# Performance work log

Hardware: AMD Instinct MI355X
Metric: run time of the kernel (lower is better)

Reference implementation:

```python
import jax, jax.numpy as jnp
import numpy as np

N_NODES = 100000
N_EDGES = 1000000
IN_CH = 64
HID = 64
NUM_GRAPHS = 1024


def gcn_conv(x, edge_index, W, b):
    # GCNConv with self-loops and symmetric normalization.
    src, dst = edge_index[0], edge_index[1]
    n = x.shape[0]
    # degree including self-loop
    deg = jax.ops.segment_sum(jnp.ones(src.shape[0], x.dtype), dst, num_segments=n) + 1.0
    dinv = jax.lax.rsqrt(deg)
    xw = x @ W  # [N, out]
    norm = dinv[src] * dinv[dst]  # per-edge 1/sqrt(d_i d_j)
    msg = xw[src] * norm[:, None]  # [E, out] gather + scale
    agg = jax.ops.segment_sum(msg, dst, num_segments=n)
    # self-loop contribution: norm = 1/deg
    return agg + xw / deg[:, None] + b


def setup_inputs() -> dict:
    key = jax.random.key(0)
    k = jax.random.split(key, 8)
    x = jax.random.normal(k[0], (N_NODES, IN_CH), dtype=jnp.float32)
    edge_index = jax.random.randint(k[1], (2, N_EDGES), 0, N_NODES, dtype=jnp.int64)
    batch = jnp.sort(jax.random.randint(k[2], (N_NODES,), 0, NUM_GRAPHS, dtype=jnp.int64))
    s1 = 1.0 / np.sqrt(IN_CH)
    s2 = 1.0 / np.sqrt(HID)
    W1 = jax.random.uniform(k[3], (IN_CH, HID), jnp.float32, -s1, s1)
    b1 = jnp.zeros((HID,), jnp.float32)
    W2 = jax.random.uniform(k[4], (HID, HID), jnp.float32, -s2, s2)
    b2 = jnp.zeros((HID,), jnp.float32)
    Wout = jax.random.uniform(k[5], (HID, 1), jnp.float32, -s2, s2)
    bout = jnp.zeros((1,), jnp.float32)
    return {"x": x, "edge_index": edge_index, "batch": batch,
            "W1": W1, "b1": b1, "W2": W2, "b2": b2, "Wout": Wout, "bout": bout}


def reference(x, edge_index, batch, W1, b1, W2, b2, Wout, bout):
    h = jax.nn.relu(gcn_conv(x, edge_index, W1, b1))
    h = jax.nn.relu(gcn_conv(h, edge_index, W2, b2))
    # global_mean_pool over batch ids
    sums = jax.ops.segment_sum(h, batch, num_segments=NUM_GRAPHS)
    cnt = jax.ops.segment_sum(jnp.ones(h.shape[0], h.dtype), batch, num_segments=NUM_GRAPHS)
    pooled = sums / jnp.maximum(cnt, 1.0)[:, None]  # [G, HID]
    return (pooled @ Wout + bout).reshape(-1)
```

## Files before the change

kernel.cpp:

```cpp
#include <hip/hip_runtime.h>
#include <hip/hip_fp16.h>

#define N_NODES   100000
#define N_EDGES   1000000
#define NPAIR     (N_NODES / 2)
#define HID       64
#define NUM_GRAPHS 1024
#define NREP      8
#define CAP       32
#define PPW       8

typedef _Float16 h16;

static __device__ __forceinline__ int pack2(float a, float b) {
    union { h16 h[2]; int i; } u;
    u.h[0] = (h16)a; u.h[1] = (h16)b;
    return u.i;
}


__global__ __launch_bounds__(256) void bucket_fill(const int* __restrict__ src,
                                                   const int* __restrict__ dst,
                                                   int* __restrict__ cnt,
                                                   int* __restrict__ ebuf) {
    int part  = blockIdx.x & 7;
    int e     = (blockIdx.x >> 3) * 256 + threadIdx.x;
    if (e >= N_EDGES) return;
    int d = dst[e];
    if (((d >> 7) & 7) != part) return;
    int p = atomicAdd(&cnt[d], 1);
    if (p < CAP) ebuf[(size_t)d * CAP + p] = src[e];
}


__global__ __launch_bounds__(256) void gemm64h(const float* __restrict__ X,
                                               const float* __restrict__ W,
                                               const int* __restrict__ cnt,
                                               h16* __restrict__ Y, int nrows) {
    __shared__ float Wl[4096];
    int t = threadIdx.x;
    #pragma unroll
    for (int i = 0; i < 4; i++) {
        int idx = (t + i * 256) * 4;
        *(float4*)(Wl + idx) = *(const float4*)(W + idx);
    }
    __syncthreads();
    int row  = blockIdx.x * 128 + (t >> 1);
    if (row >= nrows) return;
    int half = t & 1;
    float df = (float)(min(cnt[row], CAP) + 1);
    float sc = rsqrtf(df);
    const float4* xr = (const float4*)(X + (size_t)row * 64);
    float4 acc[8];
    #pragma unroll
    for (int j = 0; j < 8; j++) acc[j] = make_float4(0.f, 0.f, 0.f, 0.f);
    const float* wb = Wl + half * 32;
    #pragma unroll
    for (int k4 = 0; k4 < 16; k4++) {
        float4 xv = xr[k4];
        #pragma unroll
        for (int kk = 0; kk < 4; kk++) {
            float xk = (kk == 0) ? xv.x : (kk == 1) ? xv.y : (kk == 2) ? xv.z : xv.w;
            const float4* wr = (const float4*)(wb + (k4 * 4 + kk) * 64);
            #pragma unroll
            for (int j = 0; j < 8; j++) {
                float4 wv = wr[j];
                acc[j].x += xk * wv.x;
                acc[j].y += xk * wv.y;
                acc[j].z += xk * wv.z;
                acc[j].w += xk * wv.w;
            }
        }
    }
    int4* yr = (int4*)(Y + (size_t)row * 64 + half * 32);
    #pragma unroll
    for (int j = 0; j < 4; j++) {
        float4 a = acc[2 * j], b = acc[2 * j + 1];
        int4 o;
        o.x = pack2(a.x * sc, a.y * sc); o.y = pack2(a.z * sc, a.w * sc);
        o.z = pack2(b.x * sc, b.y * sc); o.w = pack2(b.z * sc, b.w * sc);
        yr[j] = o;
    }
}


template <int U>
static __device__ __forceinline__ float agg_chunk(const h16* __restrict__ XW,
                                                  int es, int j, int lane) {
    int ss[U]; float vv[U];
    #pragma unroll
    for (int u = 0; u < U; u++) ss[u] = __builtin_amdgcn_readlane(es, j + u);
    #pragma unroll
    for (int u = 0; u < U; u++)
        vv[u] = (float)XW[(((unsigned)ss[u]) << 6) | (unsigned)lane];
    float a = 0.f;
    #pragma unroll
    for (int u = 0; u < U; u++) a += vv[u];
    return a;
}

static __device__ __forceinline__ float agg_edges(const h16* __restrict__ XW,
                                                  int es, int deg, int lane, int base) {
    float acc = 0.f;
    int j = 0;
    for (; j + 16 <= deg; j += 16) { acc += agg_chunk<16>(XW, es, base + j, lane); }
    if (deg & 8) { acc += agg_chunk<8>(XW, es, base + j, lane); j += 8; }
    if (deg & 4) { acc += agg_chunk<4>(XW, es, base + j, lane); j += 4; }
    if (deg & 2) { acc += agg_chunk<2>(XW, es, base + j, lane); j += 2; }
    if (deg & 1) { acc += agg_chunk<1>(XW, es, base + j, lane); }
    return acc;
}

__global__ __launch_bounds__(256) void agg_gemm_relu(const h16* __restrict__ XW,
                                                     const int* __restrict__ cnt,
                                                     const int* __restrict__ ebuf,
                                                     const float* __restrict__ bias,
                                                     const float* __restrict__ W2,
                                                     h16* __restrict__ Y2) {
    __shared__ float W2q[4096];
    __shared__ float hbuf[512];
    int t = threadIdx.x;
    #pragma unroll
    for (int i = 0; i < 16; i++) {
        int L = t + i * 256;
        int k = L >> 6, c = L & 63;
        W2q[(k >> 2) * 256 + c * 4 + (k & 3)] = W2[L];
    }
    __syncthreads();
    int lane = t & 63;
    int w = t >> 6;
    float* hb0 = hbuf + w * 128;
    float* hb1 = hb0 + 64;
    float bl = bias[lane];
    int gw = blockIdx.x * 4 + w;
    int p = gw * PPW;
    if (p >= NPAIR) return;
    int pend = min(p + PPW, NPAIR);
    int   es = ebuf[p * 64 + lane];
    float s0 = (float)XW[p * 128 + lane];
    float s1 = (float)XW[p * 128 + 64 + lane];
    int2  c2 = *(const int2*)(cnt + 2 * p);
    while (p < pend) {
        int pn = p + 1;
        int esn = 0; float s0n = 0.f, s1n = 0.f; int2 c2n = make_int2(0, 0);
        if (pn < pend) {
            esn = ebuf[pn * 64 + lane];
            s0n = (float)XW[pn * 128 + lane];
            s1n = (float)XW[pn * 128 + 64 + lane];
            c2n = *(const int2*)(cnt + 2 * pn);
        }
        int deg0 = min(__builtin_amdgcn_readfirstlane(c2.x), CAP);
        int deg1 = min(__builtin_amdgcn_readfirstlane(c2.y), CAP);
        float dv0 = rsqrtf((float)(deg0 + 1));
        float dv1 = rsqrtf((float)(deg1 + 1));
        float acc0 = s0 + agg_edges(XW, es, deg0, lane, 0);
        float acc1 = s1 + agg_edges(XW, es, deg1, lane, 32);
        float h0 = fmaxf(fmaf(dv0, acc0, bl), 0.f);
        float h1 = fmaxf(fmaf(dv1, acc1, bl), 0.f);
        hb0[lane] = h0;
        hb1[lane] = h1;
        float y0 = 0.f, y1 = 0.f;
        #pragma unroll
        for (int k4 = 0; k4 < 16; k4++) {
            float4 hp0 = *(const float4*)(hb0 + k4 * 4);
            float4 hp1 = *(const float4*)(hb1 + k4 * 4);
            float4 wq  = *(const float4*)(W2q + k4 * 256 + lane * 4);
            y0 = fmaf(hp0.x, wq.x, y0); y1 = fmaf(hp1.x, wq.x, y1);
            y0 = fmaf(hp0.y, wq.y, y0); y1 = fmaf(hp1.y, wq.y, y1);
            y0 = fmaf(hp0.z, wq.z, y0); y1 = fmaf(hp1.z, wq.z, y1);
            y0 = fmaf(hp0.w, wq.w, y0); y1 = fmaf(hp1.w, wq.w, y1);
        }
        Y2[p * 128 + lane]      = (h16)(y0 * dv0);
        Y2[p * 128 + 64 + lane] = (h16)(y1 * dv1);
        es = esn; s0 = s0n; s1 = s1n; c2 = c2n;
        p = pn;
    }
}

__global__ __launch_bounds__(256) void agg_pool(const h16* __restrict__ XW,
                                                const int* __restrict__ cnt,
                                                const int* __restrict__ ebuf,
                                                const float* __restrict__ bias,
                                                const float* __restrict__ Wout,
                                                const int* __restrict__ batch,
                                                float* __restrict__ outsum) {
    int t = threadIdx.x;
    int lane = t & 63;
    int w = t >> 6;
    float bl = bias[lane];
    float wl = Wout[lane];
    int gw = blockIdx.x * 4 + w;
    int p = gw * PPW;
    if (p >= NPAIR) return;
    int pend = min(p + PPW, NPAIR);
    int   es = ebuf[p * 64 + lane];
    float s0 = (float)XW[p * 128 + lane];
    float s1 = (float)XW[p * 128 + 64 + lane];
    int2  c2 = *(const int2*)(cnt + 2 * p);
    int2  b2 = *(const int2*)(batch + 2 * p);
    while (p < pend) {
        int pn = p + 1;
        int esn = 0; float s0n = 0.f, s1n = 0.f;
        int2 c2n = make_int2(0, 0), b2n = make_int2(0, 0);
        if (pn < pend) {
            esn = ebuf[pn * 64 + lane];
            s0n = (float)XW[pn * 128 + lane];
            s1n = (float)XW[pn * 128 + 64 + lane];
            c2n = *(const int2*)(cnt + 2 * pn);
            b2n = *(const int2*)(batch + 2 * pn);
        }
        int deg0 = min(__builtin_amdgcn_readfirstlane(c2.x), CAP);
        int deg1 = min(__builtin_amdgcn_readfirstlane(c2.y), CAP);
        float dv0 = rsqrtf((float)(deg0 + 1));
        float dv1 = rsqrtf((float)(deg1 + 1));
        float acc0 = s0 + agg_edges(XW, es, deg0, lane, 0);
        float acc1 = s1 + agg_edges(XW, es, deg1, lane, 32);
        float v0 = fmaxf(fmaf(dv0, acc0, bl), 0.f) * wl;
        float v1 = fmaxf(fmaf(dv1, acc1, bl), 0.f) * wl;
        #pragma unroll
        for (int off = 32; off > 0; off >>= 1) {
            v0 += __shfl_down(v0, off, 64);
            v1 += __shfl_down(v1, off, 64);
        }
        if (lane == 0) {
            atomicAdd(&outsum[((2 * p)     & (NREP - 1)) * NUM_GRAPHS + b2.x], v0);
            atomicAdd(&outsum[((2 * p + 1) & (NREP - 1)) * NUM_GRAPHS + b2.y], v1);
        }
        es = esn; s0 = s0n; s1 = s1n; c2 = c2n; b2 = b2n;
        p = pn;
    }
}

__global__ __launch_bounds__(256) void finalize(const float* __restrict__ outsum,
                                                const int* __restrict__ batch,
                                                const float* __restrict__ bout,
                                                float* __restrict__ out) {
    int g = blockIdx.x * 256 + threadIdx.x;
    if (g >= NUM_GRAPHS) return;
    float s = 0.f;
    #pragma unroll
    for (int r = 0; r < NREP; r++) s += outsum[r * NUM_GRAPHS + g];
    int lo = 0, hi = N_NODES;
    while (lo < hi) { int mid = (lo + hi) >> 1; if (batch[mid] <  g) lo = mid + 1; else hi = mid; }
    int lo2 = lo, hi2 = N_NODES;
    while (lo2 < hi2) { int mid = (lo2 + hi2) >> 1; if (batch[mid] <= g) lo2 = mid + 1; else hi2 = mid; }
    float c = (float)max(lo2 - lo, 1);
    out[g] = s / c + bout[0];
}


extern "C" void kernel_launch(void* const* d_in, const int* in_sizes, int n_in,
                              void* d_out, int out_size, void* d_ws, size_t ws_size,
                              hipStream_t stream) {
    const float* x     = (const float*)d_in[0];
    const int*   eidx  = (const int*)d_in[1];
    const int*   batch = (const int*)d_in[2];
    const float* W1    = (const float*)d_in[3];
    const float* b1    = (const float*)d_in[4];
    const float* W2    = (const float*)d_in[5];
    const float* b2    = (const float*)d_in[6];
    const float* Wout  = (const float*)d_in[7];
    const float* bout  = (const float*)d_in[8];
    float* out = (float*)d_out;

    const int* src = eidx;
    const int* dst = eidx + N_EDGES;

    h16*   xw     = (h16*)d_ws;
    h16*   y2     = xw + (size_t)N_NODES * 64;
    int*   ebuf   = (int*)(y2 + (size_t)N_NODES * 64);
    int*   cnt    = ebuf + (size_t)N_NODES * CAP;
    float* outsum = (float*)(cnt + N_NODES);

    hipMemsetAsync(cnt, 0, (size_t)(N_NODES + NREP * NUM_GRAPHS) * sizeof(int), stream);

    const int EB  = (N_EDGES + 255) / 256;
    const int GB  = (N_NODES + 127) / 128;
    const int AGB = (NPAIR + 4 * PPW - 1) / (4 * PPW);

    bucket_fill<<<EB * 8, 256, 0, stream>>>(src, dst, cnt, ebuf);
    gemm64h<<<GB, 256, 0, stream>>>(x, W1, cnt, xw, N_NODES);
    agg_gemm_relu<<<AGB, 256, 0, stream>>>(xw, cnt, ebuf, b1, W2, y2);
    agg_pool<<<AGB, 256, 0, stream>>>(y2, cnt, ebuf, b2, Wout, batch, outsum);
    finalize<<<(NUM_GRAPHS + 255) / 256, 256, 0, stream>>>(outsum, batch, bout, out);
}
```

Baseline: 244.1 us.

## Process two node pairs per wave without loop, and vectorize W2 staging

```diff
diff --git a/kernel.cpp b/kernel.cpp
--- a/kernel.cpp
+++ b/kernel.cpp
@@ -8,7 +8,6 @@
 #define NUM_GRAPHS 1024
 #define NREP      8
 #define CAP       32
-#define PPW       8
 
 typedef _Float16 h16;
 
@@ -118,63 +117,70 @@
                                                      const float* __restrict__ W2,
                                                      h16* __restrict__ Y2) {
     __shared__ float W2q[4096];
-    __shared__ float hbuf[512];
+    __shared__ float hbuf[1024];
     int t = threadIdx.x;
     #pragma unroll
-    for (int i = 0; i < 16; i++) {
-        int L = t + i * 256;
-        int k = L >> 6, c = L & 63;
-        W2q[(k >> 2) * 256 + c * 4 + (k & 3)] = W2[L];
+    for (int i = 0; i < 4; i++) {
+        int L0 = (t + i * 256) * 4;
+        float4 wv = *(const float4*)(W2 + L0);
+        int k = L0 >> 6, c = L0 & 63;
+        float* dp = &W2q[(k >> 2) * 256 + (k & 3)];
+        dp[(c + 0) * 4] = wv.x;
+        dp[(c + 1) * 4] = wv.y;
+        dp[(c + 2) * 4] = wv.z;
+        dp[(c + 3) * 4] = wv.w;
     }
     __syncthreads();
     int lane = t & 63;
     int w = t >> 6;
-    float* hb0 = hbuf + w * 128;
-    float* hb1 = hb0 + 64;
+    float* hb = hbuf + w * 256;
     float bl = bias[lane];
     int gw = blockIdx.x * 4 + w;
-    int p = gw * PPW;
-    if (p >= NPAIR) return;
-    int pend = min(p + PPW, NPAIR);
-    int   es = ebuf[p * 64 + lane];
-    float s0 = (float)XW[p * 128 + lane];
-    float s1 = (float)XW[p * 128 + 64 + lane];
-    int2  c2 = *(const int2*)(cnt + 2 * p);
-    while (p < pend) {
-        int pn = p + 1;
-        int esn = 0; float s0n = 0.f, s1n = 0.f; int2 c2n = make_int2(0, 0);
-        if (pn < pend) {
-            esn = ebuf[pn * 64 + lane];
-            s0n = (float)XW[pn * 128 + lane];
-            s1n = (float)XW[pn * 128 + 64 + lane];
-            c2n = *(const int2*)(cnt + 2 * pn);
-        }
-        int deg0 = min(__builtin_amdgcn_readfirstlane(c2.x), CAP);
-        int deg1 = min(__builtin_amdgcn_readfirstlane(c2.y), CAP);
-        float dv0 = rsqrtf((float)(deg0 + 1));
-        float dv1 = rsqrtf((float)(deg1 + 1));
-        float acc0 = s0 + agg_edges(XW, es, deg0, lane, 0);
-        float acc1 = s1 + agg_edges(XW, es, deg1, lane, 32);
-        float h0 = fmaxf(fmaf(dv0, acc0, bl), 0.f);
-        float h1 = fmaxf(fmaf(dv1, acc1, bl), 0.f);
-        hb0[lane] = h0;
-        hb1[lane] = h1;
-        float y0 = 0.f, y1 = 0.f;
-        #pragma unroll
-        for (int k4 = 0; k4 < 16; k4++) {
-            float4 hp0 = *(const float4*)(hb0 + k4 * 4);
-            float4 hp1 = *(const float4*)(hb1 + k4 * 4);
-            float4 wq  = *(const float4*)(W2q + k4 * 256 + lane * 4);
-            y0 = fmaf(hp0.x, wq.x, y0); y1 = fmaf(hp1.x, wq.x, y1);
-            y0 = fmaf(hp0.y, wq.y, y0); y1 = fmaf(hp1.y, wq.y, y1);
-            y0 = fmaf(hp0.z, wq.z, y0); y1 = fmaf(hp1.z, wq.z, y1);
-            y0 = fmaf(hp0.w, wq.w, y0); y1 = fmaf(hp1.w, wq.w, y1);
-        }
-        Y2[p * 128 + lane]      = (h16)(y0 * dv0);
-        Y2[p * 128 + 64 + lane] = (h16)(y1 * dv1);
-        es = esn; s0 = s0n; s1 = s1n; c2 = c2n;
-        p = pn;
-    }
+    int pA = gw * 2, pB = pA + 1;
+    int   esA = ebuf[pA * 64 + lane];
+    int   esB = ebuf[pB * 64 + lane];
+    float sA0 = (float)XW[pA * 128 + lane];
+    float sA1 = (float)XW[pA * 128 + 64 + lane];
+    float sB0 = (float)XW[pB * 128 + lane];
+    float sB1 = (float)XW[pB * 128 + 64 + lane];
+    int4  c4  = *(const int4*)(cnt + 4 * gw);
+    int dA0 = min(__builtin_amdgcn_readfirstlane(c4.x), CAP);
+    int dA1 = min(__builtin_amdgcn_readfirstlane(c4.y), CAP);
+    int dB0 = min(__builtin_amdgcn_readfirstlane(c4.z), CAP);
+    int dB1 = min(__builtin_amdgcn_readfirstlane(c4.w), CAP);
+    float vA0 = rsqrtf((float)(dA0 + 1));
+    float vA1 = rsqrtf((float)(dA1 + 1));
+    float vB0 = rsqrtf((float)(dB0 + 1));
+    float vB1 = rsqrtf((float)(dB1 + 1));
+    float a0 = sA0 + agg_edges(XW, esA, dA0, lane, 0);
+    float a1 = sA1 + agg_edges(XW, esA, dA1, lane, 32);
+    float a2 = sB0 + agg_edges(XW, esB, dB0, lane, 0);
+    float a3 = sB1 + agg_edges(XW, esB, dB1, lane, 32);
+    hb[lane]       = fmaxf(fmaf(vA0, a0, bl), 0.f);
+    hb[64 + lane]  = fmaxf(fmaf(vA1, a1, bl), 0.f);
+    hb[128 + lane] = fmaxf(fmaf(vB0, a2, bl), 0.f);
+    hb[192 + lane] = fmaxf(fmaf(vB1, a3, bl), 0.f);
+    float y0 = 0.f, y1 = 0.f, y2 = 0.f, y3 = 0.f;
+    #pragma unroll
+    for (int k4 = 0; k4 < 16; k4++) {
+        float4 wq = *(const float4*)(W2q + k4 * 256 + lane * 4);
+        float4 h0 = *(const float4*)(hb + k4 * 4);
+        float4 h1 = *(const float4*)(hb + 64 + k4 * 4);
+        float4 h2 = *(const float4*)(hb + 128 + k4 * 4);
+        float4 h3 = *(const float4*)(hb + 192 + k4 * 4);
+        y0 = fmaf(h0.x, wq.x, y0); y1 = fmaf(h1.x, wq.x, y1);
+        y2 = fmaf(h2.x, wq.x, y2); y3 = fmaf(h3.x, wq.x, y3);
+        y0 = fmaf(h0.y, wq.y, y0); y1 = fmaf(h1.y, wq.y, y1);
+        y2 = fmaf(h2.y, wq.y, y2); y3 = fmaf(h3.y, wq.y, y3);
+        y0 = fmaf(h0.z, wq.z, y0); y1 = fmaf(h1.z, wq.z, y1);
+        y2 = fmaf(h2.z, wq.z, y2); y3 = fmaf(h3.z, wq.z, y3);
+        y0 = fmaf(h0.w, wq.w, y0); y1 = fmaf(h1.w, wq.w, y1);
+        y2 = fmaf(h2.w, wq.w, y2); y3 = fmaf(h3.w, wq.w, y3);
+    }
+    Y2[pA * 128 + lane]       = (h16)(y0 * vA0);
+    Y2[pA * 128 + 64 + lane]  = (h16)(y1 * vA1);
+    Y2[pB * 128 + lane]       = (h16)(y2 * vB0);
+    Y2[pB * 128 + 64 + lane]  = (h16)(y3 * vB1);
 }
 
 __global__ __launch_bounds__(256) void agg_pool(const h16* __restrict__ XW,
@@ -190,44 +196,44 @@
     float bl = bias[lane];
     float wl = Wout[lane];
     int gw = blockIdx.x * 4 + w;
-    int p = gw * PPW;
-    if (p >= NPAIR) return;
-    int pend = min(p + PPW, NPAIR);
-    int   es = ebuf[p * 64 + lane];
-    float s0 = (float)XW[p * 128 + lane];
-    float s1 = (float)XW[p * 128 + 64 + lane];
-    int2  c2 = *(const int2*)(cnt + 2 * p);
-    int2  b2 = *(const int2*)(batch + 2 * p);
-    while (p < pend) {
-        int pn = p + 1;
-        int esn = 0; float s0n = 0.f, s1n = 0.f;
-        int2 c2n = make_int2(0, 0), b2n = make_int2(0, 0);
-        if (pn < pend) {
-            esn = ebuf[pn * 64 + lane];
-            s0n = (float)XW[pn * 128 + lane];
-            s1n = (float)XW[pn * 128 + 64 + lane];
-            c2n = *(const int2*)(cnt + 2 * pn);
-            b2n = *(const int2*)(batch + 2 * pn);
-        }
-        int deg0 = min(__builtin_amdgcn_readfirstlane(c2.x), CAP);
-        int deg1 = min(__builtin_amdgcn_readfirstlane(c2.y), CAP);
-        float dv0 = rsqrtf((float)(deg0 + 1));
-        float dv1 = rsqrtf((float)(deg1 + 1));
-        float acc0 = s0 + agg_edges(XW, es, deg0, lane, 0);
-        float acc1 = s1 + agg_edges(XW, es, deg1, lane, 32);
-        float v0 = fmaxf(fmaf(dv0, acc0, bl), 0.f) * wl;
-        float v1 = fmaxf(fmaf(dv1, acc1, bl), 0.f) * wl;
-        #pragma unroll
-        for (int off = 32; off > 0; off >>= 1) {
-            v0 += __shfl_down(v0, off, 64);
-            v1 += __shfl_down(v1, off, 64);
-        }
-        if (lane == 0) {
-            atomicAdd(&outsum[((2 * p)     & (NREP - 1)) * NUM_GRAPHS + b2.x], v0);
-            atomicAdd(&outsum[((2 * p + 1) & (NREP - 1)) * NUM_GRAPHS + b2.y], v1);
-        }
-        es = esn; s0 = s0n; s1 = s1n; c2 = c2n; b2 = b2n;
-        p = pn;
+    int pA = gw * 2, pB = pA + 1;
+    int   esA = ebuf[pA * 64 + lane];
+    int   esB = ebuf[pB * 64 + lane];
+    float sA0 = (float)XW[pA * 128 + lane];
+    float sA1 = (float)XW[pA * 128 + 64 + lane];
+    float sB0 = (float)XW[pB * 128 + lane];
+    float sB1 = (float)XW[pB * 128 + 64 + lane];
+    int4  c4  = *(const int4*)(cnt + 4 * gw);
+    int4  b4  = *(const int4*)(batch + 4 * gw);
+    int dA0 = min(__builtin_amdgcn_readfirstlane(c4.x), CAP);
+    int dA1 = min(__builtin_amdgcn_readfirstlane(c4.y), CAP);
+    int dB0 = min(__builtin_amdgcn_readfirstlane(c4.z), CAP);
+    int dB1 = min(__builtin_amdgcn_readfirstlane(c4.w), CAP);
+    float vsA0 = rsqrtf((float)(dA0 + 1));
+    float vsA1 = rsqrtf((float)(dA1 + 1));
+    float vsB0 = rsqrtf((float)(dB0 + 1));
+    float vsB1 = rsqrtf((float)(dB1 + 1));
+    float a0 = sA0 + agg_edges(XW, esA, dA0, lane, 0);
+    float a1 = sA1 + agg_edges(XW, esA, dA1, lane, 32);
+    float a2 = sB0 + agg_edges(XW, esB, dB0, lane, 0);
+    float a3 = sB1 + agg_edges(XW, esB, dB1, lane, 32);
+    float v0 = fmaxf(fmaf(vsA0, a0, bl), 0.f) * wl;
+    float v1 = fmaxf(fmaf(vsA1, a1, bl), 0.f) * wl;
+    float v2 = fmaxf(fmaf(vsB0, a2, bl), 0.f) * wl;
+    float v3 = fmaxf(fmaf(vsB1, a3, bl), 0.f) * wl;
+    #pragma unroll
+    for (int off = 32; off > 0; off >>= 1) {
+        v0 += __shfl_down(v0, off, 64);
+        v1 += __shfl_down(v1, off, 64);
+        v2 += __shfl_down(v2, off, 64);
+        v3 += __shfl_down(v3, off, 64);
+    }
+    if (lane == 0) {
+        int n0 = 4 * gw;
+        atomicAdd(&outsum[((n0 + 0) & (NREP - 1)) * NUM_GRAPHS + b4.x], v0);
+        atomicAdd(&outsum[((n0 + 1) & (NREP - 1)) * NUM_GRAPHS + b4.y], v1);
+        atomicAdd(&outsum[((n0 + 2) & (NREP - 1)) * NUM_GRAPHS + b4.z], v2);
+        atomicAdd(&outsum[((n0 + 3) & (NREP - 1)) * NUM_GRAPHS + b4.w], v3);
     }
 }
 
@@ -276,7 +282,7 @@
 
     const int EB  = (N_EDGES + 255) / 256;
     const int GB  = (N_NODES + 127) / 128;
-    const int AGB = (NPAIR + 4 * PPW - 1) / (4 * PPW);
+    const int AGB = NPAIR / 8;
 
     bucket_fill<<<EB * 8, 256, 0, stream>>>(src, dst, cnt, ebuf);
     gemm64h<<<GB, 256, 0, stream>>>(x, W1, cnt, xw, N_NODES);
```

New measurement: 233.8 us. 4.2% less time.
